# Performance work log

Measured on AMD Instinct MI355X. Metric: run time of the kernel, lower is better.

## Reference

```python
import jax, jax.numpy as jnp
import numpy as np


def setup_inputs() -> dict:
    key = jax.random.key(0)
    ks = jax.random.split(key, 6)
    C = 256
    B, D, H, W = 4, 16, 16, 16
    s = 0.02
    return {
        "x": jax.random.normal(ks[0], (B, C, D, H, W), jnp.float32),
        "Wq": jax.random.normal(ks[1], (C // 8, C), jnp.float32) * s,
        "bq": jnp.zeros((C // 8,), jnp.float32),
        "Wk": jax.random.normal(ks[2], (C // 8, C), jnp.float32) * s,
        "bk": jnp.zeros((C // 8,), jnp.float32),
        "Wv": jax.random.normal(ks[3], (C, C), jnp.float32) * s,
        "bv": jnp.zeros((C,), jnp.float32),
        "gamma": jnp.zeros((1,), jnp.float32),
    }


def reference(x, Wq, bq, Wk, bk, Wv, bv, gamma):
    B, C, D, H, W = x.shape
    N = D * H * W
    xf = x.reshape(B, C, N)  # [B, C, N] flattened spatial tokens
    # 1x1 Conv3d == per-token channel matmul
    q = jnp.einsum("oc,bcn->bno", Wq, xf) + bq  # [B, N, C/8]
    k = jnp.einsum("oc,bcn->bon", Wk, xf) + bk[None, :, None]  # [B, C/8, N]
    v = jnp.einsum("oc,bcn->bon", Wv, xf) + bv[None, :, None]  # [B, C, N]
    attn = jax.nn.softmax(jnp.einsum("bnd,bdm->bnm", q, k), axis=-1)  # [B, N, N]
    # out[b,c,i] = sum_j v[b,c,j] * attn[i,j]  (bmm(value, attn^T))
    out = jnp.einsum("bcj,bij->bci", v, attn).reshape(B, C, D, H, W)
    return gamma[0] * out + x
```

## Files before the change

### kernel.cpp

```cpp
#include <hip/hip_runtime.h>
#include <math.h>

#define BB 4
#define CC 256
#define CO 32
#define NN 4096

__global__ void k0_residual(const float* __restrict__ x,
                            const float* __restrict__ gamma,
                            float* __restrict__ out) {
    if (gamma[0] != 0.0f) return;
    const float4* __restrict__ x4 = (const float4*)x;
    float4* __restrict__ o4 = (float4*)out;
    const int n4 = BB * CC * NN / 4;
    for (int i = blockIdx.x * blockDim.x + threadIdx.x; i < n4;
         i += gridDim.x * blockDim.x) {
        o4[i] = x4[i];
    }
}

__global__ void k1_qkv(const float* __restrict__ x,
                       const float* __restrict__ Wq, const float* __restrict__ bq,
                       const float* __restrict__ Wk, const float* __restrict__ bk,
                       const float* __restrict__ Wv, const float* __restrict__ bv,
                       const float* __restrict__ gamma,
                       float* __restrict__ qws, float* __restrict__ kws,
                       float* __restrict__ vws) {
    if (gamma[0] == 0.0f) return;
    const int chunks_per_b = NN / 64;
    const int b  = blockIdx.x / chunks_per_b;
    const int n0 = (blockIdx.x % chunks_per_b) * 64;
    const int t  = threadIdx.x & 63;
    const int g  = threadIdx.x >> 6;
    const int n  = n0 + t;
    const size_t xb = (size_t)b * CC * NN;

    for (int o = g; o < CO; o += 4) {
        float s = bq[o];
        for (int c = 0; c < CC; ++c)
            s += Wq[o * CC + c] * x[xb + (size_t)c * NN + n];
        qws[((size_t)b * NN + n) * CO + o] = s;
    }
    for (int o = g; o < CO; o += 4) {
        float s = bk[o];
        for (int c = 0; c < CC; ++c)
            s += Wk[o * CC + c] * x[xb + (size_t)c * NN + n];
        kws[((size_t)b * NN + n) * CO + o] = s;
    }
    for (int o = g; o < CC; o += 4) {
        float s = bv[o];
        for (int c = 0; c < CC; ++c)
            s += Wv[o * CC + c] * x[xb + (size_t)c * NN + n];
        vws[((size_t)b * NN + n) * CC + o] = s;
    }
}

__global__ void k2_attn(const float* __restrict__ x,
                        const float* __restrict__ gamma,
                        const float* __restrict__ qws,
                        const float* __restrict__ kws,
                        const float* __restrict__ vws,
                        float* __restrict__ out) {
    const float gval = gamma[0];
    if (gval == 0.0f) return;

    __shared__ float qs[16][CO];
    __shared__ float ps[16][64];
    __shared__ float alpha_s[16];
    __shared__ float l_s[16];

    const int tiles_per_b = NN / 16;
    const int tid = threadIdx.x;
    const int si = tid >> 4, jg = tid & 15;
    const int pi = tid & 15, cb = (tid >> 4) * 16;

    for (int rep = 0; rep < 2; ++rep) {
        const int tile = blockIdx.x * 2 + rep;
        const int b  = tile / tiles_per_b;
        const int i0 = (tile % tiles_per_b) * 16;

        for (int idx = tid; idx < 16 * CO; idx += 256) {
            int r = idx / CO, d = idx % CO;
            qs[r][d] = qws[((size_t)b * NN + i0 + r) * CO + d];
        }
        __syncthreads();

        float m = -INFINITY, l = 0.0f;
        float acc[16];
        #pragma unroll
        for (int r = 0; r < 16; ++r) acc[r] = 0.0f;

        for (int jc = 0; jc < NN / 64; ++jc) {
            const int j0 = jc * 64;
            float sv[4];
            #pragma unroll
            for (int qq = 0; qq < 4; ++qq) {
                const int j = j0 + jg * 4 + qq;
                const float* krow = &kws[((size_t)b * NN + j) * CO];
                float s = 0.0f;
                #pragma unroll
                for (int d = 0; d < CO; ++d) s += qs[si][d] * krow[d];
                sv[qq] = s;
            }
            float cm = fmaxf(fmaxf(sv[0], sv[1]), fmaxf(sv[2], sv[3]));
            #pragma unroll
            for (int msk = 1; msk < 16; msk <<= 1)
                cm = fmaxf(cm, __shfl_xor(cm, msk));
            const float m_new = fmaxf(m, cm);
            const float alpha = expf(m - m_new);
            float cs = 0.0f;
            #pragma unroll
            for (int qq = 0; qq < 4; ++qq) {
                sv[qq] = expf(sv[qq] - m_new);
                cs += sv[qq];
            }
            #pragma unroll
            for (int msk = 1; msk < 16; msk <<= 1)
                cs += __shfl_xor(cs, msk);
            l = l * alpha + cs;
            m = m_new;
            #pragma unroll
            for (int qq = 0; qq < 4; ++qq) ps[si][jg * 4 + qq] = sv[qq];
            if (jg == 0) alpha_s[si] = alpha;
            __syncthreads();

            const float a = alpha_s[pi];
            #pragma unroll
            for (int r = 0; r < 16; ++r) acc[r] *= a;
            for (int j = 0; j < 64; ++j) {
                const float p = ps[pi][j];
                const float* vrow = &vws[((size_t)b * NN + j0 + j) * CC + cb];
                #pragma unroll
                for (int r = 0; r < 16; ++r) acc[r] += p * vrow[r];
            }
            __syncthreads();
        }

        if (jg == 0) l_s[si] = l;
        __syncthreads();
        const float linv = 1.0f / l_s[pi];
        #pragma unroll
        for (int r = 0; r < 16; ++r) {
            const size_t oidx = ((size_t)b * CC + cb + r) * NN + i0 + pi;
            out[oidx] = gval * (acc[r] * linv) + x[oidx];
        }
        __syncthreads();
    }
}

extern "C" void kernel_launch(void* const* d_in, const int* in_sizes, int n_in,
                              void* d_out, int out_size, void* d_ws, size_t ws_size,
                              hipStream_t stream) {
    (void)in_sizes; (void)n_in; (void)out_size; (void)ws_size;
    const float* x     = (const float*)d_in[0];
    const float* Wq    = (const float*)d_in[1];
    const float* bq    = (const float*)d_in[2];
    const float* Wk    = (const float*)d_in[3];
    const float* bk    = (const float*)d_in[4];
    const float* Wv    = (const float*)d_in[5];
    const float* bv    = (const float*)d_in[6];
    const float* gamma = (const float*)d_in[7];
    float* out = (float*)d_out;

    float* qws = (float*)d_ws;
    float* kws = qws + (size_t)BB * NN * CO;
    float* vws = kws + (size_t)BB * NN * CO;

    k0_residual<<<2048, 256, 0, stream>>>(x, gamma, out);
    k1_qkv<<<BB * (NN / 64), 256, 0, stream>>>(x, Wq, bq, Wk, bk, Wv, bv,
                                               gamma, qws, kws, vws);
    k2_attn<<<(BB * (NN / 16)) / 2, 256, 0, stream>>>(x, gamma, qws, kws, vws, out);
}
```

Measured before the change: 83.94 us.

## Fuse residual copy, QKV projection and attention into a single kernel

The residual-copy, QKV-projection and attention kernels are merged into one launch. When gamma is zero, the fused kernel only does the float4 copy of x into the output. Otherwise each tile recomputes its Q, K and V projections into shared memory instead of reading them from a workspace. This removes two kernel launches and the workspace round trip. The price is that every tile redundantly recomputes the K and V projections over the full sequence when gamma is nonzero, which adds a very large amount of extra compute on that path.

```diff
diff --git a/kernel.cpp b/kernel.cpp
--- a/kernel.cpp
+++ b/kernel.cpp
@@ -5,169 +5,150 @@
 #define CC 256
 #define CO 32
 #define NN 4096
+#define NTILES (BB * (NN / 16))
+#define GRID 2048
 
-__global__ void k0_residual(const float* __restrict__ x,
-                            const float* __restrict__ gamma,
-                            float* __restrict__ out) {
-    if (gamma[0] != 0.0f) return;
-    const float4* __restrict__ x4 = (const float4*)x;
-    float4* __restrict__ o4 = (float4*)out;
-    const int n4 = BB * CC * NN / 4;
-    for (int i = blockIdx.x * blockDim.x + threadIdx.x; i < n4;
-         i += gridDim.x * blockDim.x) {
-        o4[i] = x4[i];
+__global__ __launch_bounds__(256) void fused_sa3d(
+    const float* __restrict__ x,
+    const float* __restrict__ Wq, const float* __restrict__ bq,
+    const float* __restrict__ Wk, const float* __restrict__ bk,
+    const float* __restrict__ Wv, const float* __restrict__ bv,
+    const float* __restrict__ gamma,
+    float* __restrict__ out) {
+    const float gval = gamma[0];
+    const int tid = threadIdx.x;
+
+    if (gval == 0.0f) {
+        const float4* __restrict__ x4 = (const float4*)x;
+        float4* __restrict__ o4 = (float4*)out;
+        const int n4 = BB * CC * NN / 4;
+        for (int i = blockIdx.x * 256 + tid; i < n4; i += GRID * 256)
+            o4[i] = x4[i];
+        return;
     }
-}
 
-__global__ void k1_qkv(const float* __restrict__ x,
-                       const float* __restrict__ Wq, const float* __restrict__ bq,
-                       const float* __restrict__ Wk, const float* __restrict__ bk,
-                       const float* __restrict__ Wv, const float* __restrict__ bv,
-                       const float* __restrict__ gamma,
-                       float* __restrict__ qws, float* __restrict__ kws,
-                       float* __restrict__ vws) {
-    if (gamma[0] == 0.0f) return;
-    const int chunks_per_b = NN / 64;
-    const int b  = blockIdx.x / chunks_per_b;
-    const int n0 = (blockIdx.x % chunks_per_b) * 64;
-    const int t  = threadIdx.x & 63;
-    const int g  = threadIdx.x >> 6;
-    const int n  = n0 + t;
-    const size_t xb = (size_t)b * CC * NN;
-
-    for (int o = g; o < CO; o += 4) {
-        float s = bq[o];
-        for (int c = 0; c < CC; ++c)
-            s += Wq[o * CC + c] * x[xb + (size_t)c * NN + n];
-        qws[((size_t)b * NN + n) * CO + o] = s;
-    }
-    for (int o = g; o < CO; o += 4) {
-        float s = bk[o];
-        for (int c = 0; c < CC; ++c)
-            s += Wk[o * CC + c] * x[xb + (size_t)c * NN + n];
-        kws[((size_t)b * NN + n) * CO + o] = s;
-    }
-    for (int o = g; o < CC; o += 4) {
-        float s = bv[o];
-        for (int c = 0; c < CC; ++c)
-            s += Wv[o * CC + c] * x[xb + (size_t)c * NN + n];
-        vws[((size_t)b * NN + n) * CC + o] = s;
-    }
-}
-
-__global__ void k2_attn(const float* __restrict__ x,
-                        const float* __restrict__ gamma,
-                        const float* __restrict__ qws,
-                        const float* __restrict__ kws,
-                        const float* __restrict__ vws,
-                        float* __restrict__ out) {
-    const float gval = gamma[0];
-    if (gval == 0.0f) return;
+    if (blockIdx.x >= NTILES) return;
 
     __shared__ float qs[16][CO];
+    __shared__ float ks[64][CO];
     __shared__ float ps[16][64];
+    __shared__ float vsb[64][64];
     __shared__ float alpha_s[16];
     __shared__ float l_s[16];
 
-    const int tiles_per_b = NN / 16;
-    const int tid = threadIdx.x;
+    const int tile = blockIdx.x;
+    const int b  = tile / (NN / 16);
+    const int i0 = (tile % (NN / 16)) * 16;
+    const size_t xb = (size_t)b * CC * NN;
+
     const int si = tid >> 4, jg = tid & 15;
     const int pi = tid & 15, cb = (tid >> 4) * 16;
 
-    for (int rep = 0; rep < 2; ++rep) {
-        const int tile = blockIdx.x * 2 + rep;
-        const int b  = tile / tiles_per_b;
-        const int i0 = (tile % tiles_per_b) * 16;
+    for (int idx = tid; idx < 16 * CO; idx += 256) {
+        const int r = idx >> 5, o = idx & 31;
+        float s = bq[o];
+        for (int c = 0; c < CC; ++c)
+            s += Wq[o * CC + c] * x[xb + (size_t)c * NN + i0 + r];
+        qs[r][o] = s;
+    }
+    __syncthreads();
 
-        for (int idx = tid; idx < 16 * CO; idx += 256) {
-            int r = idx / CO, d = idx % CO;
-            qs[r][d] = qws[((size_t)b * NN + i0 + r) * CO + d];
+    float m = -INFINITY, l = 0.0f;
+    float acc[16];
+    #pragma unroll
+    for (int r = 0; r < 16; ++r) acc[r] = 0.0f;
+
+    for (int jc = 0; jc < NN / 64; ++jc) {
+        const int j0 = jc * 64;
+
+        for (int idx = tid; idx < 64 * CO; idx += 256) {
+            const int j = idx >> 5, o = idx & 31;
+            float s = bk[o];
+            for (int c = 0; c < CC; ++c)
+                s += Wk[o * CC + c] * x[xb + (size_t)c * NN + j0 + j];
+            ks[j][o] = s;
         }
         __syncthreads();
 
-        float m = -INFINITY, l = 0.0f;
-        float acc[16];
+        float sv[4];
         #pragma unroll
-        for (int r = 0; r < 16; ++r) acc[r] = 0.0f;
+        for (int qq = 0; qq < 4; ++qq) {
+            const int j = jg * 4 + qq;
+            float s = 0.0f;
+            #pragma unroll
+            for (int d = 0; d < CO; ++d) s += qs[si][d] * ks[j][d];
+            sv[qq] = s;
+        }
+        float cm = fmaxf(fmaxf(sv[0], sv[1]), fmaxf(sv[2], sv[3]));
+        #pragma unroll
+        for (int msk = 1; msk < 16; msk <<= 1)
+            cm = fmaxf(cm, __shfl_xor(cm, msk));
+        const float m_new = fmaxf(m, cm);
+        const float alpha = expf(m - m_new);
+        float cs = 0.0f;
+        #pragma unroll
+        for (int qq = 0; qq < 4; ++qq) {
+            sv[qq] = expf(sv[qq] - m_new);
+            cs += sv[qq];
+        }
+        #pragma unroll
+        for (int msk = 1; msk < 16; msk <<= 1)
+            cs += __shfl_xor(cs, msk);
+        l = l * alpha + cs;
+        m = m_new;
+        #pragma unroll
+        for (int qq = 0; qq < 4; ++qq) ps[si][jg * 4 + qq] = sv[qq];
+        if (jg == 0) alpha_s[si] = alpha;
+        __syncthreads();
 
-        for (int jc = 0; jc < NN / 64; ++jc) {
-            const int j0 = jc * 64;
-            float sv[4];
-            #pragma unroll
-            for (int qq = 0; qq < 4; ++qq) {
-                const int j = j0 + jg * 4 + qq;
-                const float* krow = &kws[((size_t)b * NN + j) * CO];
-                float s = 0.0f;
-                #pragma unroll
-                for (int d = 0; d < CO; ++d) s += qs[si][d] * krow[d];
-                sv[qq] = s;
+        const float a = alpha_s[pi];
+        #pragma unroll
+        for (int r = 0; r < 16; ++r) acc[r] *= a;
+        for (int g = 0; g < 4; ++g) {
+            for (int idx = tid; idx < 64 * 64; idx += 256) {
+                const int j = idx >> 6, co = idx & 63;
+                const int c = g * 64 + co;
+                float s = bv[c];
+                for (int cc = 0; cc < CC; ++cc)
+                    s += Wv[c * CC + cc] * x[xb + (size_t)cc * NN + j0 + j];
+                vsb[j][co] = s;
             }
-            float cm = fmaxf(fmaxf(sv[0], sv[1]), fmaxf(sv[2], sv[3]));
-            #pragma unroll
-            for (int msk = 1; msk < 16; msk <<= 1)
-                cm = fmaxf(cm, __shfl_xor(cm, msk));
-            const float m_new = fmaxf(m, cm);
-            const float alpha = expf(m - m_new);
-            float cs = 0.0f;
-            #pragma unroll
-            for (int qq = 0; qq < 4; ++qq) {
-                sv[qq] = expf(sv[qq] - m_new);
-                cs += sv[qq];
-            }
-            #pragma unroll
-            for (int msk = 1; msk < 16; msk <<= 1)
-                cs += __shfl_xor(cs, msk);
-            l = l * alpha + cs;
-            m = m_new;
-            #pragma unroll
-            for (int qq = 0; qq < 4; ++qq) ps[si][jg * 4 + qq] = sv[qq];
-            if (jg == 0) alpha_s[si] = alpha;
             __syncthreads();
-
-            const float a = alpha_s[pi];
-            #pragma unroll
-            for (int r = 0; r < 16; ++r) acc[r] *= a;
-            for (int j = 0; j < 64; ++j) {
-                const float p = ps[pi][j];
-                const float* vrow = &vws[((size_t)b * NN + j0 + j) * CC + cb];
-                #pragma unroll
-                for (int r = 0; r < 16; ++r) acc[r] += p * vrow[r];
+            if ((cb >> 6) == g) {
+                const int cbl = cb & 63;
+                for (int j = 0; j < 64; ++j) {
+                    const float p = ps[pi][j];
+                    #pragma unroll
+                    for (int r = 0; r < 16; ++r) acc[r] += p * vsb[j][cbl + r];
+                }
             }
             __syncthreads();
         }
+    }
 
-        if (jg == 0) l_s[si] = l;
-        __syncthreads();
-        const float linv = 1.0f / l_s[pi];
-        #pragma unroll
-        for (int r = 0; r < 16; ++r) {
-            const size_t oidx = ((size_t)b * CC + cb + r) * NN + i0 + pi;
-            out[oidx] = gval * (acc[r] * linv) + x[oidx];
-        }
-        __syncthreads();
+    if (jg == 0) l_s[si] = l;
+    __syncthreads();
+    const float linv = 1.0f / l_s[pi];
+    #pragma unroll
+    for (int r = 0; r < 16; ++r) {
+        const size_t oidx = ((size_t)b * CC + cb + r) * NN + i0 + pi;
+        out[oidx] = gval * (acc[r] * linv) + x[oidx];
     }
 }
 
 extern "C" void kernel_launch(void* const* d_in, const int* in_sizes, int n_in,
                               void* d_out, int out_size, void* d_ws, size_t ws_size,
                               hipStream_t stream) {
-    (void)in_sizes; (void)n_in; (void)out_size; (void)ws_size;
+    (void)in_sizes; (void)n_in; (void)out_size; (void)d_ws; (void)ws_size;
     const float* x     = (const float*)d_in[0];
     const float* Wq    = (const float*)d_in[1];
     const float* bq    = (const float*)d_in[2];
+    const float* bk    = (const float*)d_in[4];
     const float* Wk    = (const float*)d_in[3];
-    const float* bk    = (const float*)d_in[4];
     const float* Wv    = (const float*)d_in[5];
     const float* bv    = (const float*)d_in[6];
     const float* gamma = (const float*)d_in[7];
     float* out = (float*)d_out;
 
-    float* qws = (float*)d_ws;
-    float* kws = qws + (size_t)BB * NN * CO;
-    float* vws = kws + (size_t)BB * NN * CO;
-
-    k0_residual<<<2048, 256, 0, stream>>>(x, gamma, out);
-    k1_qkv<<<BB * (NN / 64), 256, 0, stream>>>(x, Wq, bq, Wk, bk, Wv, bv,
-                                               gamma, qws, kws, vws);
-    k2_attn<<<(BB * (NN / 16)) / 2, 256, 0, stream>>>(x, gamma, qws, kws, vws, out);
+    fused_sa3d<<<GRID, 256, 0, stream>>>(x, Wq, bq, Wk, bk, Wv, bv, gamma, out);
 }
```

After: 81.28 us. 1.03x faster.
